# Performance work log

Measured on AMD Instinct MI355X. Metric: run time of the kernel, lower is better.

The kernel has to match this reference:

```python
import jax, jax.numpy as jnp
import numpy as np

B, N, NQ, C = 4, 16384, 1024, 128
NS = 64          # nsample
RADIUS = 0.3     # ball-query fallback radius


def setup_inputs() -> dict:
    key = jax.random.key(0)
    k1, k2, k3, k4 = jax.random.split(key, 4)
    key_xyz = jax.random.uniform(k1, (B, N, 3), dtype=jnp.float32)
    key_features = jax.random.normal(k2, (B, C, N), dtype=jnp.float32)
    centers = jax.random.uniform(k3, (B, NQ, 3), dtype=jnp.float32)
    # box sizes L/H/W in [0.05, 0.25]
    sizes = 0.05 + 0.2 * jax.random.uniform(k4, (B, NQ, 3), dtype=jnp.float32)
    query_xyz = jnp.concatenate([centers, sizes], axis=-1)
    return {"key_xyz": key_xyz, "key_features": key_features, "query_xyz": query_xyz}


def _box_group(key_xyz, key_features, query_xyz):
    centers = query_xyz[:, :, :3]              # [B,nq,3]
    half = 0.5 * query_xyz[:, :, 3:]           # [B,nq,3] half box extents

    # per-query per-key absolute offsets: [B,nq,N,3]
    d = jnp.abs(key_xyz[:, None, :, :] - centers[:, :, None, :])
    inside = jnp.all(d <= half[:, :, None, :], axis=-1)      # [B,nq,N] AABB test
    dist2 = jnp.sum(d * d, axis=-1)                          # [B,nq,N]

    # ball-query fallback for queries whose box contains no point
    has_box = jnp.any(inside, axis=-1)                       # [B,nq]
    sel = jnp.where(has_box[..., None], inside, dist2 <= RADIUS * RADIUS)

    # first NS selected indices (stable sort puts selected points first,
    # preserving ascending key index order -> deterministic box_query semantics)
    order = jnp.argsort((~sel).astype(jnp.int32), axis=-1)[:, :, :NS]  # [B,nq,NS]

    count = jnp.minimum(jnp.sum(sel, axis=-1), NS)           # [B,nq]
    pad = jnp.arange(NS)[None, None, :] >= count[..., None]  # True = padded slot
    idx = jnp.where(pad, 0, order)                           # pad with index 0
    mask = pad.at[:, :, 0].set(False)                        # cuda path: mask[...,0]=False

    # gathers
    g_xyz = jax.vmap(lambda k, i: k[i])(key_xyz, idx)        # [B,nq,NS,3]
    g_xyz = g_xyz - centers[:, :, None, :]                   # recenter on query
    grouped_xyz = jnp.transpose(g_xyz, (0, 3, 1, 2))         # [B,3,nq,NS]
    grouped_feat = jax.vmap(lambda f, i: f[:, i])(key_features, idx)  # [B,C,nq,NS]
    return grouped_xyz, grouped_feat, mask


def reference(key_xyz, key_features, query_xyz):
    return _box_group(key_xyz, key_features, query_xyz)
```

## Files before the change

kernel.cpp:

```cpp
#include <hip/hip_runtime.h>

#pragma clang fp contract(off)

#define B_  4
#define N_  16384
#define NQ_ 1024
#define C_  128
#define NS_ 64
#define G_  16
#define NCELL_ 4096
#define MAXCELLS_ 224
#define SELCAP_ 1024

#define OFF_FEAT   ((size_t)0)
#define SZ_FEAT    ((size_t)B_*N_*C_*4)
#define OFF_COUNTS (OFF_FEAT + SZ_FEAT)
#define OFF_CURSOR (OFF_COUNTS + (size_t)B_*NCELL_*4)
#define OFF_CINFO  (OFF_CURSOR + (size_t)B_*NCELL_*4)
#define OFF_PLIST4 (OFF_CINFO + (size_t)B_*NCELL_*8)
#define WS_NEED    (OFF_PLIST4 + (size_t)B_*N_*16)

__device__ __forceinline__ int cell_of(float x, float y, float z) {
    int ix = (int)(x * (float)G_); ix = min(G_ - 1, max(0, ix));
    int iy = (int)(y * (float)G_); iy = min(G_ - 1, max(0, iy));
    int iz = (int)(z * (float)G_); iz = min(G_ - 1, max(0, iz));
    return ix + (iy << 4) + (iz << 8);
}

__device__ __forceinline__ int cell_lo(float c, float h) {
    float lo = c - h;
    lo -= fabsf(lo) * 3e-7f + 1e-9f;
    return max(0, (int)floorf(lo * (float)G_));
}
__device__ __forceinline__ int cell_hi(float c, float h) {
    float hi = c + h;
    hi += fabsf(hi) * 3e-7f + 1e-9f;
    return min(G_ - 1, (int)floorf(hi * (float)G_));
}

__global__ __launch_bounds__(256) void bin_count_k(const float* __restrict__ key_xyz,
                                                   int* __restrict__ counts) {
    int id = blockIdx.x * 256 + threadIdx.x;
    int b = id >> 14, n = id & (N_ - 1);
    const float* p = key_xyz + ((size_t)b * N_ + n) * 3;
    int cid = cell_of(p[0], p[1], p[2]);
    atomicAdd(&counts[(b << 12) + cid], 1);
}

__global__ __launch_bounds__(1024) void scan_k(const int* __restrict__ counts,
                                               int2* __restrict__ cinfo,
                                               int* __restrict__ cursor) {
    __shared__ int wsum[16];
    int b = blockIdx.x, t = threadIdx.x;
    int wave = t >> 6, lane = t & 63;
    int base = b << 12;
    int c0 = t << 2;
    int v0 = counts[base + c0 + 0], v1 = counts[base + c0 + 1];
    int v2 = counts[base + c0 + 2], v3 = counts[base + c0 + 3];
    int s = v0 + v1 + v2 + v3;
    int x = s;
#pragma unroll
    for (int o = 1; o < 64; o <<= 1) {
        int v = __shfl_up(x, (unsigned)o);
        if (lane >= o) x += v;
    }
    if (lane == 63) wsum[wave] = x;
    __syncthreads();
    if (t < 16) {
        int y = wsum[t];
#pragma unroll
        for (int o = 1; o < 16; o <<= 1) {
            int v = __shfl_up(y, (unsigned)o);
            if (t >= o) y += v;
        }
        wsum[t] = y;
    }
    __syncthreads();
    int off = (wave ? wsum[wave - 1] : 0) + x - s;
    int e0 = off, e1 = e0 + v0, e2 = e1 + v1, e3 = e2 + v2;
    cinfo[base + c0 + 0] = make_int2(v0, e0); cursor[base + c0 + 0] = e0;
    cinfo[base + c0 + 1] = make_int2(v1, e1); cursor[base + c0 + 1] = e1;
    cinfo[base + c0 + 2] = make_int2(v2, e2); cursor[base + c0 + 2] = e2;
    cinfo[base + c0 + 3] = make_int2(v3, e3); cursor[base + c0 + 3] = e3;
}

#define TBLK_ (B_ * (C_/32) * (N_/32))
__global__ __launch_bounds__(256) void scatter_transpose_k(
    const float* __restrict__ key_xyz, const float* __restrict__ key_feat,
    int* __restrict__ cursor, float4* __restrict__ plist4,
    float* __restrict__ feat_t)
{
    __shared__ float ttile[32][33];
    int t = threadIdx.x;
    if (blockIdx.x < TBLK_) {
        int id2 = blockIdx.x;
        int b   = id2 >> 11;
        int rem = id2 & 2047;
        int c0  = (rem >> 9) * 32;
        int n0  = (rem & 511) * 32;
        int x = t & 31, y = t >> 5;
#pragma unroll
        for (int k = 0; k < 4; ++k)
            ttile[y + 8*k][x] = __builtin_nontemporal_load(
                &key_feat[((size_t)b * C_ + c0 + y + 8*k) * N_ + n0 + x]);
        __syncthreads();
#pragma unroll
        for (int k = 0; k < 4; ++k)
            feat_t[((size_t)b * N_ + n0 + y + 8*k) * C_ + c0 + x] = ttile[x][y + 8*k];
        return;
    }
    int id = (blockIdx.x - TBLK_) * 256 + t;
    int b = id >> 14, n = id & (N_ - 1);
    const float* p = key_xyz + ((size_t)b * N_ + n) * 3;
    float x = p[0], y = p[1], z = p[2];
    int cid = cell_of(x, y, z);
    int pos = atomicAdd(&cursor[(b << 12) + cid], 1);
    plist4[(b << 14) + pos] = make_float4(x, y, z, __int_as_float(n));
}

__global__ __launch_bounds__(512) void selgather_k(
    const float* __restrict__ key_xyz, const float* __restrict__ query,
    const int2* __restrict__ cinfo, const float4* __restrict__ plist4,
    const float* __restrict__ feat_t,
    float* __restrict__ out_xyz, float* __restrict__ out_feat,
    float* __restrict__ out_mask)
{
    __shared__ int   s_ccnt[MAXCELLS_];
    __shared__ int   s_cstart[MAXCELLS_];
    __shared__ int   s_pref[MAXCELLS_ + 1];
    __shared__ int   s_sel[SELCAP_];
    __shared__ int   s_scnt;
    __shared__ int   s_list[8][NS_];
    __shared__ int   s_cnt8[8];
    __shared__ int   s_idx[NS_];
    __shared__ int   s_count;
    __shared__ float tile[NS_][65];

    int i    = blockIdx.x;
    int xcd  = i & 7;
    int b    = xcd >> 1;
    int q    = ((i >> 3) << 1) | (xcd & 1);
    int bq   = (b << 10) | q;
    int t    = threadIdx.x;
    int wave = t >> 6, lane = t & 63;

    const float* qp = query + (size_t)bq * 6;
    float cx = qp[0], cy = qp[1], cz = qp[2];
    float hx = 0.5f * qp[3], hy = 0.5f * qp[4], hz = 0.5f * qp[5];
    const float* kb = key_xyz + (size_t)b * N_ * 3;

    if (t == 0) s_scnt = 0;

    int ilox = cell_lo(cx, hx), ihix = cell_hi(cx, hx);
    int iloy = cell_lo(cy, hy), ihiy = cell_hi(cy, hy);
    int iloz = cell_lo(cz, hz), ihiz = cell_hi(cz, hz);
    int nx = ihix - ilox + 1, ny = ihiy - iloy + 1, nz = ihiz - iloz + 1;
    int ncells = nx * ny * nz;

    const int2* ci = cinfo + (b << 12);
    for (int cc = t; cc < ncells; cc += 512) {
        int iz = cc / (nx * ny);
        int r  = cc - iz * (nx * ny);
        int iy = r / nx;
        int ix = r - iy * nx;
        int cid = (ilox + ix) + ((iloy + iy) << 4) + ((iloz + iz) << 8);
        int2 v = ci[cid];
        s_ccnt[cc]   = v.x;
        s_cstart[cc] = v.y;
    }
    __syncthreads();

    if (wave == 0) {
        int run = 0;
        for (int base = 0; base < ncells; base += 64) {
            int x = (base + lane < ncells) ? s_ccnt[base + lane] : 0;
            int own = x;
#pragma unroll
            for (int o = 1; o < 64; o <<= 1) {
                int v = __shfl_up(x, (unsigned)o);
                if (lane >= o) x += v;
            }
            if (base + lane < ncells) s_pref[base + lane] = run + x - own;
            run += __shfl(x, 63);
        }
        if (lane == 0) s_pref[ncells] = run;
    }
    __syncthreads();

    int total = s_pref[ncells];
    const float4* pl = plist4 + ((size_t)b << 14);
    for (int ii = t; ii < total; ii += 512) {
        int lo = 0, hi = ncells;
        while (hi - lo > 1) {
            int mid = (lo + hi) >> 1;
            if (s_pref[mid] <= ii) lo = mid; else hi = mid;
        }
        float4 p = pl[s_cstart[lo] + (ii - s_pref[lo])];
        float dx = fabsf(p.x - cx);
        float dy = fabsf(p.y - cy);
        float dz = fabsf(p.z - cz);
        if (dx <= hx && dy <= hy && dz <= hz) {
            int pos = atomicAdd(&s_scnt, 1);
            if (pos < SELCAP_) s_sel[pos] = __float_as_int(p.w);
        }
    }
    __syncthreads();
    int scnt = min(s_scnt, SELCAP_);

    if (scnt > 0) {
        int count = min(scnt, NS_);
        if (scnt <= NS_) {
            if (wave == 0) {
                int v = (lane < scnt) ? s_sel[lane] : 0x7fffffff;
#pragma unroll
                for (int k = 2; k <= 64; k <<= 1) {
                    for (int j = k >> 1; j > 0; j >>= 1) {
                        int pv = __shfl_xor(v, (unsigned)j);
                        bool dir   = (lane & k) == 0;
                        bool lower = (lane & j) == 0;
                        int mn = min(v, pv), mx = max(v, pv);
                        v = dir ? (lower ? mn : mx) : (lower ? mx : mn);
                    }
                }
                s_idx[lane] = (lane < count) ? v : 0;
                if (lane == 0) s_count = count;
            }
        } else if (scnt <= 512) {
            int nw = (scnt + 63) >> 6;
            int base = wave << 6;
            int v = (base + lane < scnt) ? s_sel[base + lane] : 0x7fffffff;
#pragma unroll
            for (int k = 2; k <= 64; k <<= 1) {
                for (int j = k >> 1; j > 0; j >>= 1) {
                    int pv = __shfl_xor(v, (unsigned)j);
                    bool dir   = (lane & k) == 0;
                    bool lower = (lane & j) == 0;
                    int mn = min(v, pv), mx = max(v, pv);
                    v = dir ? (lower ? mn : mx) : (lower ? mx : mn);
                }
            }
            s_sel[base + lane] = v;
            __syncthreads();
            int e = s_sel[t];
            if (t < (nw << 6) && e != 0x7fffffff) {
                int r = lane;
#pragma unroll
                for (int w = 0; w < 8; ++w) {
                    if (w == wave || w >= nw) continue;
                    int bw = w << 6;
                    int pos = 0;
#pragma unroll
                    for (int s2 = 32; s2 >= 1; s2 >>= 1)
                        if (s_sel[bw + pos + s2 - 1] < e) pos += s2;
                    if (s_sel[bw + pos] < e) ++pos;
                    r += pos;
                }
                if (r < NS_) s_idx[r] = e;
            }
            if (t == 0) s_count = NS_;
        } else {
            int m = NS_;
            while (m < scnt) m <<= 1;
            for (int ii = t; ii < m; ii += 512)
                if (ii >= scnt) s_sel[ii] = 0x7fffffff;
            __syncthreads();
            for (int k = 2; k <= m; k <<= 1) {
                for (int j = k >> 1; j > 0; j >>= 1) {
                    for (int ii = t; ii < m; ii += 512) {
                        int ixj = ii ^ j;
                        if (ixj > ii) {
                            int va = s_sel[ii], vb = s_sel[ixj];
                            bool up = ((ii & k) == 0);
                            if ((va > vb) == up) { s_sel[ii] = vb; s_sel[ixj] = va; }
                        }
                    }
                    __syncthreads();
                }
            }
            if (t < NS_) s_idx[t] = (t < count) ? s_sel[t] : 0;
            if (t == 0)  s_count = count;
        }
    } else {
        const float R2 = (float)(0.3 * 0.3);
        const int seg = N_ / 8;
        int n0s = wave * seg;
        unsigned long long ltm = (1ull << lane) - 1ull;
        int cnt = 0;
        for (int it = 0; it < seg / 64; ++it) {
            int n = n0s + it * 64 + lane;
            float dx = kb[3*n + 0] - cx;
            float dy = kb[3*n + 1] - cy;
            float dz = kb[3*n + 2] - cz;
            float d2 = dx*dx + dy*dy + dz*dz;
            bool r = d2 <= R2;
            unsigned long long mm = __ballot(r);
            if (r) {
                int p = cnt + __popcll(mm & ltm);
                if (p < NS_) s_list[wave][p] = n;
            }
            cnt += __popcll(mm);
            if (cnt >= NS_) break;
        }
        if (lane == 0) s_cnt8[wave] = cnt;
        __syncthreads();
        if (wave == 0) {
            int tot = 0;
#pragma unroll
            for (int w = 0; w < 8; ++w) tot += s_cnt8[w];
            int count = min(tot, NS_);
            int j = lane;
            int idx = 0;
            if (j < count) {
                int w = 0, rem = j;
                while (rem >= s_cnt8[w]) { rem -= s_cnt8[w]; ++w; }
                idx = s_list[w][rem];
            }
            s_idx[j] = idx;
            if (lane == 0) s_count = count;
        }
    }
    __syncthreads();

    int count = s_count;
    if (t < NS_) {
        int j = t, idx = s_idx[j];
        out_mask[(size_t)bq * NS_ + j] = (j >= count && j > 0) ? 1.0f : 0.0f;
        float px = kb[3*idx + 0] - cx;
        float py = kb[3*idx + 1] - cy;
        float pz = kb[3*idx + 2] - cz;
        size_t xb = ((size_t)b * 3) * NQ_ * NS_ + (size_t)q * NS_ + j;
        out_xyz[xb]                       = px;
        out_xyz[xb +     (size_t)NQ_*NS_] = py;
        out_xyz[xb + 2 * (size_t)NQ_*NS_] = pz;
    }

    const float4* ft4 = (const float4*)feat_t + (size_t)b * N_ * (C_ / 4);
    float* ob = out_feat + (size_t)b * C_ * NQ_ * NS_ + (size_t)q * NS_;
#pragma unroll
    for (int chunk = 0; chunk < 2; ++chunk) {
#pragma unroll
        for (int k = 0; k < 2; ++k) {
            int u  = t + k * 512;
            int j  = u >> 4;
            int c4 = u & 15;
            float4 v = ft4[(size_t)s_idx[j] * (C_ / 4) + chunk * 16 + c4];
            tile[j][c4*4 + 0] = v.x;
            tile[j][c4*4 + 1] = v.y;
            tile[j][c4*4 + 2] = v.z;
            tile[j][c4*4 + 3] = v.w;
        }
        __syncthreads();
#pragma unroll
        for (int r = 0; r < 8; ++r) {
            int cl = wave + r * 8;
            __builtin_nontemporal_store(tile[lane][cl],
                &ob[(size_t)(chunk * 64 + cl) * (NQ_ * NS_) + lane]);
        }
        __syncthreads();
    }
}

__global__ __launch_bounds__(256) void select_lin_k(
    const float* __restrict__ key_xyz, const float* __restrict__ query,
    int* __restrict__ idx_out, float* __restrict__ out_xyz,
    float* __restrict__ out_mask)
{
    int bq = blockIdx.x;
    int b  = bq >> 10;
    int q  = bq & (NQ_ - 1);
    int t    = threadIdx.x;
    int wave = t >> 6;
    int lane = t & 63;

    __shared__ int s_list[4][NS_];
    __shared__ int s_cnt[4];

    const float* qp = query + (size_t)bq * 6;
    float cx = qp[0], cy = qp[1], cz = qp[2];
    float hx = 0.5f * qp[3], hy = 0.5f * qp[4], hz = 0.5f * qp[5];
    const float* kb = key_xyz + (size_t)b * N_ * 3;

    const int seg = N_ / 4;
    int n0 = wave * seg;
    unsigned long long lt = (1ull << lane) - 1ull;

    int cnt = 0;
    for (int it = 0; it < seg / 64; ++it) {
        int n = n0 + it * 64 + lane;
        float dx = fabsf(kb[3*n + 0] - cx);
        float dy = fabsf(kb[3*n + 1] - cy);
        float dz = fabsf(kb[3*n + 2] - cz);
        bool inside = (dx <= hx) && (dy <= hy) && (dz <= hz);
        unsigned long long m = __ballot(inside);
        if (inside) {
            int p = cnt + __popcll(m & lt);
            if (p < NS_) s_list[wave][p] = n;
        }
        cnt += __popcll(m);
        if (cnt >= NS_) break;
    }
    if (lane == 0) s_cnt[wave] = cnt;
    __syncthreads();

    int ti = s_cnt[0] + s_cnt[1] + s_cnt[2] + s_cnt[3];
    if (ti == 0) {
        const float R2 = (float)(0.3 * 0.3);
        cnt = 0;
        for (int it = 0; it < seg / 64; ++it) {
            int n = n0 + it * 64 + lane;
            float dx = kb[3*n + 0] - cx;
            float dy = kb[3*n + 1] - cy;
            float dz = kb[3*n + 2] - cz;
            float d2 = dx*dx + dy*dy + dz*dz;
            bool r = d2 <= R2;
            unsigned long long m = __ballot(r);
            if (r) {
                int p = cnt + __popcll(m & lt);
                if (p < NS_) s_list[wave][p] = n;
            }
            cnt += __popcll(m);
            if (cnt >= NS_) break;
        }
        if (lane == 0) s_cnt[wave] = cnt;
    }
    __syncthreads();

    if (wave == 0) {
        int c0s = min(s_cnt[0], NS_);
        int c1s = min(s_cnt[1], NS_);
        int c2s = min(s_cnt[2], NS_);
        int tot   = s_cnt[0] + s_cnt[1] + s_cnt[2] + s_cnt[3];
        int count = min(tot, NS_);
        int j = lane;
        int idx = 0;
        if (j < count) {
            int o1 = c0s, o2 = o1 + c1s, o3 = o2 + c2s;
            if      (j < o1) idx = s_list[0][j];
            else if (j < o2) idx = s_list[1][j - o1];
            else if (j < o3) idx = s_list[2][j - o2];
            else             idx = s_list[3][j - o3];
        }
        idx_out[(size_t)bq * NS_ + j] = idx;
        out_mask[(size_t)bq * NS_ + j] = (j >= count && j > 0) ? 1.0f : 0.0f;
        float px = kb[3*idx + 0] - cx;
        float py = kb[3*idx + 1] - cy;
        float pz = kb[3*idx + 2] - cz;
        size_t xb = ((size_t)b * 3) * NQ_ * NS_ + (size_t)q * NS_ + j;
        out_xyz[xb]                       = px;
        out_xyz[xb +     (size_t)NQ_*NS_] = py;
        out_xyz[xb + 2 * (size_t)NQ_*NS_] = pz;
    }
}

__global__ __launch_bounds__(256) void gather_direct_k(
    const int* __restrict__ idx_in, const float* __restrict__ key_feat,
    float* __restrict__ out_feat)
{
    int bq = blockIdx.x;
    int b  = bq >> 10;
    int q  = bq & (NQ_ - 1);
    int t    = threadIdx.x;
    int wave = t >> 6;
    int lane = t & 63;
    __shared__ int s_idx[NS_];
    if (t < NS_) s_idx[t] = idx_in[(size_t)bq * NS_ + t];
    __syncthreads();
    const float* fb = key_feat + (size_t)b * C_ * N_;
    float* ob = out_feat + (size_t)b * C_ * NQ_ * NS_ + (size_t)q * NS_;
    int idx = s_idx[lane];
    for (int c = wave; c < C_; c += 4)
        ob[(size_t)c * NQ_ * NS_ + lane] = fb[(size_t)c * N_ + idx];
}

extern "C" void kernel_launch(void* const* d_in, const int* in_sizes, int n_in,
                              void* d_out, int out_size, void* d_ws, size_t ws_size,
                              hipStream_t stream) {
    const float* key_xyz  = (const float*)d_in[0];
    const float* key_feat = (const float*)d_in[1];
    const float* query    = (const float*)d_in[2];

    float* out      = (float*)d_out;
    float* out_xyz  = out;
    float* out_feat = out + (size_t)B_ * 3 * NQ_ * NS_;
    float* out_mask = out_feat + (size_t)B_ * C_ * NQ_ * NS_;

    char* ws = (char*)d_ws;
    float*  ft      = (float*)(ws + OFF_FEAT);
    int*    counts  = (int*)(ws + OFF_COUNTS);
    int*    cursor  = (int*)(ws + OFF_CURSOR);
    int2*   cinfo   = (int2*)(ws + OFF_CINFO);
    float4* plist4  = (float4*)(ws + OFF_PLIST4);

    if (ws_size >= WS_NEED) {
        hipMemsetAsync(counts, 0, (size_t)B_ * NCELL_ * 4, stream);
        bin_count_k<<<dim3(B_ * N_ / 256), dim3(256), 0, stream>>>(key_xyz, counts);
        scan_k<<<dim3(B_), dim3(1024), 0, stream>>>(counts, cinfo, cursor);
        scatter_transpose_k<<<dim3(TBLK_ + B_ * N_ / 256), dim3(256), 0, stream>>>(
            key_xyz, key_feat, cursor, plist4, ft);
        selgather_k<<<dim3(B_ * NQ_), dim3(512), 0, stream>>>(
            key_xyz, query, cinfo, plist4, ft, out_xyz, out_feat, out_mask);
    } else {
        int* d_idx = (int*)d_ws;
        select_lin_k<<<dim3(B_ * NQ_), dim3(256), 0, stream>>>(
            key_xyz, query, d_idx, out_xyz, out_mask);
        gather_direct_k<<<dim3(B_ * NQ_), dim3(256), 0, stream>>>(
            d_idx, key_feat, out_feat);
    }
}
```

Baseline: 199.3 us.

## Vectorize feature transpose and gather with swizzled LDS tile and early loads

```diff
diff --git a/kernel.cpp b/kernel.cpp
--- a/kernel.cpp
+++ b/kernel.cpp
@@ -11,6 +11,8 @@
 #define NCELL_ 4096
 #define MAXCELLS_ 224
 #define SELCAP_ 1024
+
+typedef float vf4 __attribute__((ext_vector_type(4)));
 
 #define OFF_FEAT   ((size_t)0)
 #define SZ_FEAT    ((size_t)B_*N_*C_*4)
@@ -84,38 +86,54 @@
     cinfo[base + c0 + 3] = make_int2(v3, e3); cursor[base + c0 + 3] = e3;
 }
 
-#define TBLK_ (B_ * (C_/32) * (N_/32))
+#define TTBLK_ (B_ * (C_/64) * (N_/64))
 __global__ __launch_bounds__(256) void scatter_transpose_k(
     const float* __restrict__ key_xyz, const float* __restrict__ key_feat,
     int* __restrict__ cursor, float4* __restrict__ plist4,
     float* __restrict__ feat_t)
 {
-    __shared__ float ttile[32][33];
+    __shared__ float ttile[64][65];
     int t = threadIdx.x;
-    if (blockIdx.x < TBLK_) {
-        int id2 = blockIdx.x;
-        int b   = id2 >> 11;
-        int rem = id2 & 2047;
-        int c0  = (rem >> 9) * 32;
-        int n0  = (rem & 511) * 32;
-        int x = t & 31, y = t >> 5;
-#pragma unroll
-        for (int k = 0; k < 4; ++k)
-            ttile[y + 8*k][x] = __builtin_nontemporal_load(
-                &key_feat[((size_t)b * C_ + c0 + y + 8*k) * N_ + n0 + x]);
-        __syncthreads();
-#pragma unroll
-        for (int k = 0; k < 4; ++k)
-            feat_t[((size_t)b * N_ + n0 + y + 8*k) * C_ + c0 + x] = ttile[x][y + 8*k];
+    if (blockIdx.x < 256) {
+        int id = blockIdx.x * 256 + t;
+        int b = id >> 14, n = id & (N_ - 1);
+        const float* p = key_xyz + ((size_t)b * N_ + n) * 3;
+        float x = p[0], y = p[1], z = p[2];
+        int cid = cell_of(x, y, z);
+        int pos = atomicAdd(&cursor[(b << 12) + cid], 1);
+        plist4[(b << 14) + pos] = make_float4(x, y, z, __int_as_float(n));
         return;
     }
-    int id = (blockIdx.x - TBLK_) * 256 + t;
-    int b = id >> 14, n = id & (N_ - 1);
-    const float* p = key_xyz + ((size_t)b * N_ + n) * 3;
-    float x = p[0], y = p[1], z = p[2];
-    int cid = cell_of(x, y, z);
-    int pos = atomicAdd(&cursor[(b << 12) + cid], 1);
-    plist4[(b << 14) + pos] = make_float4(x, y, z, __int_as_float(n));
+    int id2 = blockIdx.x - 256;
+    int b   = id2 >> 9;
+    int rem = id2 & 511;
+    int cb  = rem >> 8;
+    int nb  = rem & 255;
+    {
+        int nf = t & 15, cr = t >> 4;
+#pragma unroll
+        for (int k = 0; k < 4; ++k) {
+            int c = cr + 16 * k;
+            vf4 v = __builtin_nontemporal_load(
+                (const vf4*)&key_feat[((size_t)(b * C_ + cb * 64 + c)) * N_ + nb * 64 + 4 * nf]);
+            ttile[c][4*nf + 0] = v.x; ttile[c][4*nf + 1] = v.y;
+            ttile[c][4*nf + 2] = v.z; ttile[c][4*nf + 3] = v.w;
+        }
+    }
+    __syncthreads();
+    {
+        int cf = t & 15, nr = t >> 4;
+#pragma unroll
+        for (int k = 0; k < 4; ++k) {
+            int n = nr + 16 * k;
+            vf4 w;
+            w.x = ttile[4*cf + 0][n];
+            w.y = ttile[4*cf + 1][n];
+            w.z = ttile[4*cf + 2][n];
+            w.w = ttile[4*cf + 3][n];
+            *(vf4*)&feat_t[((size_t)b * N_ + nb * 64 + n) * C_ + cb * 64 + 4 * cf] = w;
+        }
+    }
 }
 
 __global__ __launch_bounds__(512) void selgather_k(
@@ -125,16 +143,18 @@
     float* __restrict__ out_xyz, float* __restrict__ out_feat,
     float* __restrict__ out_mask)
 {
-    __shared__ int   s_ccnt[MAXCELLS_];
-    __shared__ int   s_cstart[MAXCELLS_];
-    __shared__ int   s_pref[MAXCELLS_ + 1];
-    __shared__ int   s_sel[SELCAP_];
-    __shared__ int   s_scnt;
-    __shared__ int   s_list[8][NS_];
-    __shared__ int   s_cnt8[8];
-    __shared__ int   s_idx[NS_];
-    __shared__ int   s_count;
-    __shared__ float tile[NS_][65];
+    union SMem {
+        struct {
+            int ccnt[MAXCELLS_];
+            int cstart[MAXCELLS_];
+            int pref[MAXCELLS_ + 1];
+            int sel[SELCAP_];
+            int list[8][NS_];
+        } s;
+        float tile[NS_][132];
+    };
+    __shared__ __align__(16) SMem u;
+    __shared__ int s_scnt, s_count, s_cnt8[8], s_idx[NS_];
 
     int i    = blockIdx.x;
     int xcd  = i & 7;
@@ -165,43 +185,43 @@
         int ix = r - iy * nx;
         int cid = (ilox + ix) + ((iloy + iy) << 4) + ((iloz + iz) << 8);
         int2 v = ci[cid];
-        s_ccnt[cc]   = v.x;
-        s_cstart[cc] = v.y;
+        u.s.ccnt[cc]   = v.x;
+        u.s.cstart[cc] = v.y;
     }
     __syncthreads();
 
     if (wave == 0) {
         int run = 0;
         for (int base = 0; base < ncells; base += 64) {
-            int x = (base + lane < ncells) ? s_ccnt[base + lane] : 0;
+            int x = (base + lane < ncells) ? u.s.ccnt[base + lane] : 0;
             int own = x;
 #pragma unroll
             for (int o = 1; o < 64; o <<= 1) {
                 int v = __shfl_up(x, (unsigned)o);
                 if (lane >= o) x += v;
             }
-            if (base + lane < ncells) s_pref[base + lane] = run + x - own;
+            if (base + lane < ncells) u.s.pref[base + lane] = run + x - own;
             run += __shfl(x, 63);
         }
-        if (lane == 0) s_pref[ncells] = run;
-    }
-    __syncthreads();
-
-    int total = s_pref[ncells];
+        if (lane == 0) u.s.pref[ncells] = run;
+    }
+    __syncthreads();
+
+    int total = u.s.pref[ncells];
     const float4* pl = plist4 + ((size_t)b << 14);
     for (int ii = t; ii < total; ii += 512) {
         int lo = 0, hi = ncells;
         while (hi - lo > 1) {
             int mid = (lo + hi) >> 1;
-            if (s_pref[mid] <= ii) lo = mid; else hi = mid;
-        }
-        float4 p = pl[s_cstart[lo] + (ii - s_pref[lo])];
+            if (u.s.pref[mid] <= ii) lo = mid; else hi = mid;
+        }
+        float4 p = pl[u.s.cstart[lo] + (ii - u.s.pref[lo])];
         float dx = fabsf(p.x - cx);
         float dy = fabsf(p.y - cy);
         float dz = fabsf(p.z - cz);
         if (dx <= hx && dy <= hy && dz <= hz) {
             int pos = atomicAdd(&s_scnt, 1);
-            if (pos < SELCAP_) s_sel[pos] = __float_as_int(p.w);
+            if (pos < SELCAP_) u.s.sel[pos] = __float_as_int(p.w);
         }
     }
     __syncthreads();
@@ -211,7 +231,7 @@
         int count = min(scnt, NS_);
         if (scnt <= NS_) {
             if (wave == 0) {
-                int v = (lane < scnt) ? s_sel[lane] : 0x7fffffff;
+                int v = (lane < scnt) ? u.s.sel[lane] : 0x7fffffff;
 #pragma unroll
                 for (int k = 2; k <= 64; k <<= 1) {
                     for (int j = k >> 1; j > 0; j >>= 1) {
@@ -228,7 +248,7 @@
         } else if (scnt <= 512) {
             int nw = (scnt + 63) >> 6;
             int base = wave << 6;
-            int v = (base + lane < scnt) ? s_sel[base + lane] : 0x7fffffff;
+            int v = (base + lane < scnt) ? u.s.sel[base + lane] : 0x7fffffff;
 #pragma unroll
             for (int k = 2; k <= 64; k <<= 1) {
                 for (int j = k >> 1; j > 0; j >>= 1) {
@@ -239,9 +259,9 @@
                     v = dir ? (lower ? mn : mx) : (lower ? mx : mn);
                 }
             }
-            s_sel[base + lane] = v;
+            u.s.sel[base + lane] = v;
             __syncthreads();
-            int e = s_sel[t];
+            int e = u.s.sel[t];
             if (t < (nw << 6) && e != 0x7fffffff) {
                 int r = lane;
 #pragma unroll
@@ -251,8 +271,8 @@
                     int pos = 0;
 #pragma unroll
                     for (int s2 = 32; s2 >= 1; s2 >>= 1)
-                        if (s_sel[bw + pos + s2 - 1] < e) pos += s2;
-                    if (s_sel[bw + pos] < e) ++pos;
+                        if (u.s.sel[bw + pos + s2 - 1] < e) pos += s2;
+                    if (u.s.sel[bw + pos] < e) ++pos;
                     r += pos;
                 }
                 if (r < NS_) s_idx[r] = e;
@@ -262,22 +282,22 @@
             int m = NS_;
             while (m < scnt) m <<= 1;
             for (int ii = t; ii < m; ii += 512)
-                if (ii >= scnt) s_sel[ii] = 0x7fffffff;
+                if (ii >= scnt) u.s.sel[ii] = 0x7fffffff;
             __syncthreads();
             for (int k = 2; k <= m; k <<= 1) {
                 for (int j = k >> 1; j > 0; j >>= 1) {
                     for (int ii = t; ii < m; ii += 512) {
                         int ixj = ii ^ j;
                         if (ixj > ii) {
-                            int va = s_sel[ii], vb = s_sel[ixj];
+                            int va = u.s.sel[ii], vb = u.s.sel[ixj];
                             bool up = ((ii & k) == 0);
-                            if ((va > vb) == up) { s_sel[ii] = vb; s_sel[ixj] = va; }
+                            if ((va > vb) == up) { u.s.sel[ii] = vb; u.s.sel[ixj] = va; }
                         }
                     }
                     __syncthreads();
                 }
             }
-            if (t < NS_) s_idx[t] = (t < count) ? s_sel[t] : 0;
+            if (t < NS_) s_idx[t] = (t < count) ? u.s.sel[t] : 0;
             if (t == 0)  s_count = count;
         }
     } else {
@@ -296,7 +316,7 @@
             unsigned long long mm = __ballot(r);
             if (r) {
                 int p = cnt + __popcll(mm & ltm);
-                if (p < NS_) s_list[wave][p] = n;
+                if (p < NS_) u.s.list[wave][p] = n;
             }
             cnt += __popcll(mm);
             if (cnt >= NS_) break;
@@ -313,13 +333,22 @@
             if (j < count) {
                 int w = 0, rem = j;
                 while (rem >= s_cnt8[w]) { rem -= s_cnt8[w]; ++w; }
-                idx = s_list[w][rem];
+                idx = u.s.list[w][rem];
             }
             s_idx[j] = idx;
             if (lane == 0) s_count = count;
         }
     }
     __syncthreads();
+
+    const float4* ft4 = (const float4*)feat_t + (size_t)b * N_ * (C_ / 4);
+    int c4 = t & 31;
+    int j0 = t >> 5;
+    int r0 = s_idx[j0], r1 = s_idx[j0 + 16], r2 = s_idx[j0 + 32], r3 = s_idx[j0 + 48];
+    float4 v0 = ft4[(size_t)r0 * (C_/4) + c4];
+    float4 v1 = ft4[(size_t)r1 * (C_/4) + c4];
+    float4 v2 = ft4[(size_t)r2 * (C_/4) + c4];
+    float4 v3 = ft4[(size_t)r3 * (C_/4) + c4];
 
     int count = s_count;
     if (t < NS_) {
@@ -334,29 +363,25 @@
         out_xyz[xb + 2 * (size_t)NQ_*NS_] = pz;
     }
 
-    const float4* ft4 = (const float4*)feat_t + (size_t)b * N_ * (C_ / 4);
+    *(float4*)&u.tile[j0     ][4 * (c4 ^ (((j0     ) >> 2) & 7))] = v0;
+    *(float4*)&u.tile[j0 + 16][4 * (c4 ^ (((j0 + 16) >> 2) & 7))] = v1;
+    *(float4*)&u.tile[j0 + 32][4 * (c4 ^ (((j0 + 32) >> 2) & 7))] = v2;
+    *(float4*)&u.tile[j0 + 48][4 * (c4 ^ (((j0 + 48) >> 2) & 7))] = v3;
+    __syncthreads();
+
     float* ob = out_feat + (size_t)b * C_ * NQ_ * NS_ + (size_t)q * NS_;
-#pragma unroll
-    for (int chunk = 0; chunk < 2; ++chunk) {
-#pragma unroll
-        for (int k = 0; k < 2; ++k) {
-            int u  = t + k * 512;
-            int j  = u >> 4;
-            int c4 = u & 15;
-            float4 v = ft4[(size_t)s_idx[j] * (C_ / 4) + chunk * 16 + c4];
-            tile[j][c4*4 + 0] = v.x;
-            tile[j][c4*4 + 1] = v.y;
-            tile[j][c4*4 + 2] = v.z;
-            tile[j][c4*4 + 3] = v.w;
-        }
-        __syncthreads();
-#pragma unroll
-        for (int r = 0; r < 8; ++r) {
-            int cl = wave + r * 8;
-            __builtin_nontemporal_store(tile[lane][cl],
-                &ob[(size_t)(chunk * 64 + cl) * (NQ_ * NS_) + lane]);
-        }
-        __syncthreads();
+    int jg = t & 15, cb0 = t >> 4;
+#pragma unroll
+    for (int k = 0; k < 4; ++k) {
+        int cc = cb0 + 32 * k;
+        int ch = cc >> 2, cl = cc & 3;
+        int key = jg & 7;
+        vf4 w;
+        w.x = u.tile[4*jg + 0][4 * (ch ^ key) + cl];
+        w.y = u.tile[4*jg + 1][4 * (ch ^ key) + cl];
+        w.z = u.tile[4*jg + 2][4 * (ch ^ key) + cl];
+        w.w = u.tile[4*jg + 3][4 * (ch ^ key) + cl];
+        __builtin_nontemporal_store(w, (vf4*)&ob[(size_t)cc * (NQ_ * NS_) + 4 * jg]);
     }
 }
 
@@ -492,10 +517,10 @@
     float4* plist4  = (float4*)(ws + OFF_PLIST4);
 
     if (ws_size >= WS_NEED) {
-        hipMemsetAsync(counts, 0, (size_t)B_ * NCELL_ * 4, stream);
+        (void)hipMemsetAsync(counts, 0, (size_t)B_ * NCELL_ * 4, stream);
         bin_count_k<<<dim3(B_ * N_ / 256), dim3(256), 0, stream>>>(key_xyz, counts);
         scan_k<<<dim3(B_), dim3(1024), 0, stream>>>(counts, cinfo, cursor);
-        scatter_transpose_k<<<dim3(TBLK_ + B_ * N_ / 256), dim3(256), 0, stream>>>(
+        scatter_transpose_k<<<dim3(256 + TTBLK_), dim3(256), 0, stream>>>(
             key_xyz, key_feat, cursor, plist4, ft);
         selgather_k<<<dim3(B_ * NQ_), dim3(512), 0, stream>>>(
             key_xyz, query, cinfo, plist4, ft, out_xyz, out_feat, out_mask);
```

Result: no change. 197.1 us (-1.1%).
